# Kernel optimization log

Measured on AMD Instinct MI355X. Metric: run time of the kernel, lower is better.

## Reference

```python
import jax, jax.numpy as jnp
import numpy as np
from jax import lax

B, S, H, T = 64, 512, 1024, 67


def setup_inputs() -> dict:
    key = jax.random.key(0)
    ks = jax.random.split(key, 8)
    hidden = jax.random.normal(ks[0], (B, S, H), jnp.float32)
    labels = jax.random.randint(ks[1], (B, S), 0, T)
    lengths = jax.random.randint(ks[2], (B,), S // 2, S + 1)
    mask = (jnp.arange(S)[None, :] < lengths[:, None]).astype(jnp.int32)  # prefix mask, mask[:,0]=1
    W = jax.random.normal(ks[3], (H, T), jnp.float32) * 0.02
    b = jnp.zeros((T,), jnp.float32)
    start_trans = jax.random.uniform(ks[4], (T,), jnp.float32, -0.1, 0.1)
    end_trans = jax.random.uniform(ks[5], (T,), jnp.float32, -0.1, 0.1)
    trans = jax.random.uniform(ks[6], (T, T), jnp.float32, -0.1, 0.1)
    return dict(hidden=hidden, labels=labels, mask=mask, W=W, b=b,
                start_trans=start_trans, end_trans=end_trans, trans=trans)


def _crf_llh(em, tags, mask, start_trans, end_trans, trans):
    # em: (B,S,T), tags: (B,S) int, mask: (B,S) bool. torchcrf log-likelihood per sequence.
    maskf = mask.astype(em.dtype)
    # numerator: score of the gold path
    em_tag = jnp.take_along_axis(em, tags[:, :, None], axis=2)[:, :, 0]       # (B,S)
    num = start_trans[tags[:, 0]] + em_tag[:, 0]
    trans_tag = trans[tags[:, :-1], tags[:, 1:]]                              # (B,S-1)
    num = num + jnp.sum((trans_tag + em_tag[:, 1:]) * maskf[:, 1:], axis=1)
    last_idx = jnp.sum(mask.astype(jnp.int32), axis=1) - 1                    # (B,)
    last_tags = jnp.take_along_axis(tags, last_idx[:, None], axis=1)[:, 0]
    num = num + end_trans[last_tags]
    # denominator: log partition via forward algorithm (scan over time)
    def step(score, x):
        em_i, m_i = x  # (B,T), (B,)
        nxt = jax.nn.logsumexp(score[:, :, None] + trans[None] + em_i[:, None, :], axis=1)
        return jnp.where(m_i[:, None], nxt, score), None
    init = start_trans[None, :] + em[:, 0]
    score, _ = lax.scan(step, init, (em[:, 1:].transpose(1, 0, 2), mask[:, 1:].T))
    denom = jax.nn.logsumexp(score + end_trans[None, :], axis=1)
    return num - denom


def _viterbi(em, mask, start_trans, end_trans, trans):
    # returns best tag sequence (B,S), padded positions set to 0
    n_tags = em.shape[-1]
    ident = jnp.arange(n_tags)[None, :]
    def fwd(score, x):
        em_i, m_i = x  # (B,T), (B,)
        cand = score[:, :, None] + trans[None]                                # (B,T,T)
        idx = jnp.argmax(cand, axis=1)                                        # (B,T)
        nxt = jnp.max(cand, axis=1) + em_i
        score = jnp.where(m_i[:, None], nxt, score)
        idx = jnp.where(m_i[:, None], idx, ident)  # identity link on padded steps
        return score, idx
    init = start_trans[None, :] + em[:, 0]
    score, hist = lax.scan(fwd, init, (em[:, 1:].transpose(1, 0, 2), mask[:, 1:].T))
    best = jnp.argmax(score + end_trans[None, :], axis=1)                     # (B,)
    def back(carry, h):  # carry = tag at t+1, h = hist[t]: (B,T)
        prev = jnp.take_along_axis(h, carry[:, None], axis=1)[:, 0]
        return prev, prev
    _, ys = lax.scan(back, best, hist, reverse=True)                          # (S-1,B) tags[0..S-2]
    tags = jnp.concatenate([ys.transpose(1, 0), best[:, None]], axis=1)       # (B,S)
    return jnp.where(mask, tags, 0)


def reference(hidden, labels, mask, W, b, start_trans, end_trans, trans):
    maskb = mask.astype(bool)
    # dropout is identity in eval mode
    em = jnp.einsum('bsh,ht->bst', jax.nn.leaky_relu(hidden, 0.01), W) + b     # token_scores
    llh = _crf_llh(em, labels, maskb, start_trans, end_trans, trans)
    loss = -jnp.sum(llh) / em.shape[0]
    tags = _viterbi(em, maskb, start_trans, end_trans, trans)
    return loss, tags, em
```

## Files before the change

### kernel.cpp

```cpp
#include <hip/hip_runtime.h>

#define Bn 64
#define Sn 512
#define Hn 1024
#define Tn 67

#define LOG2E 1.4426950408889634f
#define LN2   0.6931471805599453f

__global__ __launch_bounds__(256) void gemm_em(
    const float* __restrict__ hidden, const float* __restrict__ W,
    const float* __restrict__ bias, float* __restrict__ em,
    float* __restrict__ out)
{
    __shared__ __align__(16) float hs[64][36];
    __shared__ __align__(16) float wt[80][36];

    const int tid = threadIdx.x;
    const int tx = tid & 15, ty = tid >> 4;
    const int row0 = blockIdx.x * 64;

    if (blockIdx.x == 0 && tid == 0) out[0] = 0.0f;

    float acc[4][5];
#pragma unroll
    for (int u = 0; u < 4; ++u)
#pragma unroll
        for (int v = 0; v < 5; ++v) acc[u][v] = 0.f;

    for (int kc = 0; kc < Hn; kc += 32) {
#pragma unroll
        for (int l = 0; l < 2; ++l) {
            int idx = tid + l * 256;
            int r = idx >> 3, kq = (idx & 7) << 2;
            float4 v = *reinterpret_cast<const float4*>(
                &hidden[(size_t)(row0 + r) * Hn + kc + kq]);
            v.x = v.x > 0.f ? v.x : 0.01f * v.x;
            v.y = v.y > 0.f ? v.y : 0.01f * v.y;
            v.z = v.z > 0.f ? v.z : 0.01f * v.z;
            v.w = v.w > 0.f ? v.w : 0.01f * v.w;
            *reinterpret_cast<float4*>(&hs[r][kq]) = v;
        }
        for (int idx = tid; idx < 32 * Tn; idx += 256) {
            int k = idx / Tn;
            int t = idx - k * Tn;
            wt[t][k] = W[(size_t)(kc + k) * Tn + t];
        }
        __syncthreads();

#pragma unroll
        for (int k0 = 0; k0 < 32; k0 += 4) {
            float4 hv[4], wv[5];
#pragma unroll
            for (int u = 0; u < 4; ++u)
                hv[u] = *reinterpret_cast<float4*>(&hs[ty + 16 * u][k0]);
#pragma unroll
            for (int v = 0; v < 5; ++v)
                wv[v] = *reinterpret_cast<float4*>(&wt[tx + 16 * v][k0]);
#pragma unroll
            for (int u = 0; u < 4; ++u)
#pragma unroll
                for (int v = 0; v < 5; ++v) {
                    acc[u][v] = fmaf(hv[u].x, wv[v].x, acc[u][v]);
                    acc[u][v] = fmaf(hv[u].y, wv[v].y, acc[u][v]);
                    acc[u][v] = fmaf(hv[u].z, wv[v].z, acc[u][v]);
                    acc[u][v] = fmaf(hv[u].w, wv[v].w, acc[u][v]);
                }
        }
        __syncthreads();
    }

#pragma unroll
    for (int v = 0; v < 5; ++v) {
        int c = tx + 16 * v;
        if (c < Tn) {
            float bb = bias[c];
#pragma unroll
            for (int u = 0; u < 4; ++u) {
                int row = row0 + ty + 16 * u;
                em[(size_t)row * Tn + c] = acc[u][v] + bb;
            }
        }
    }
}

__device__ __forceinline__ unsigned long long shflx64(unsigned long long v, int m) {
    unsigned int lo = (unsigned int)v, hi = (unsigned int)(v >> 32);
    lo = __shfl_xor(lo, m);
    hi = __shfl_xor(hi, m);
    return ((unsigned long long)hi << 32) | lo;
}

__device__ __forceinline__ unsigned long long packkey(float v, int idx) {
    unsigned int b = __float_as_uint(v);
    unsigned int s = b ^ (unsigned int)(((int)b >> 31) | 0x80000000);
    return ((unsigned long long)s << 32) | (unsigned int)(127 - idx);
}

__device__ __forceinline__ float unpackval(unsigned long long key) {
    unsigned int s = (unsigned int)(key >> 32);
    unsigned int b = s ^ (unsigned int)((~(int)s >> 31) | 0x80000000);
    return __uint_as_float(b);
}

__global__ __launch_bounds__(192) void crf_scan3(
    const float* __restrict__ em, const int* __restrict__ labels,
    const int* __restrict__ mask, const float* __restrict__ startT,
    const float* __restrict__ endT, const float* __restrict__ trans,
    float* __restrict__ out)
{
    __shared__ __align__(16) float emC[2][1088];
    __shared__ __align__(16) float emV[2][1088];
    __shared__ int maskC[Sn];
    __shared__ int maskV[Sn];
    __shared__ __align__(16) float pb[2][72];
    __shared__ __align__(16) float vb[2][72];
    __shared__ unsigned char hist[Sn - 1][68];
    __shared__ int tg[Sn];
    __shared__ float numSh;
    __shared__ int lenSh;

    const int tid = threadIdx.x;
    const int wid = tid >> 6;
    const int lane = tid & 63;
    const int b = blockIdx.x;
    const float* emg = em + (size_t)b * Sn * Tn;
    const int u2 = lane < 3 ? lane : 2;
    const int st2 = 64 + u2;

    if (wid == 0) {
#pragma unroll
        for (int i = 0; i < 8; ++i)
            maskC[lane + i * 64] = mask[b * Sn + lane + i * 64];

        float Ec1[68], Ec2[68];
#pragma unroll
        for (int i = 0; i < Tn; ++i) {
            Ec1[i] = exp2f(trans[i * Tn + lane] * LOG2E);
            Ec2[i] = exp2f(trans[i * Tn + st2] * LOG2E);
        }
        Ec1[67] = 0.f; Ec2[67] = 0.f;

        float sreg[17];
#pragma unroll
        for (int i = 0; i < 17; ++i) { int idx = lane + i * 64; if (idx > 1071) idx = 1071; sreg[i] = emg[idx]; }
#pragma unroll
        for (int i = 0; i < 17; ++i) {
            int idx = lane + i * 64;
            if (idx < 1072) { int s = idx / 67; emC[0][s * 68 + (idx - s * 67)] = sreg[i]; }
        }
#pragma unroll
        for (int i = 0; i < 17; ++i) { int idx = lane + i * 64; if (idx > 1071) idx = 1071; sreg[i] = emg[1072 + idx]; }

        if (lane == 0) { pb[0][67] = 0.f; pb[1][67] = 0.f; }

        float sc1 = startT[lane] + emC[0][lane];
        float sc2 = startT[st2] + emC[0][st2];
        float M = __shfl(sc1, 0);
        float p1 = exp2f((sc1 - M) * LOG2E);
        float p2 = exp2f((sc2 - M) * LOG2E);
        pb[0][lane] = p1;
        if (lane < 3) pb[0][64 + lane] = p2;
        float Mprev = M;

        for (int t = 1; t < Sn; ++t) {
            const int cb = (t >> 4) & 1;
            if ((t & 15) == 0) {
                const int k = t >> 4;
#pragma unroll
                for (int i = 0; i < 17; ++i) {
                    int idx = lane + i * 64;
                    if (idx < 1072) { int s = idx / 67; emC[cb][s * 68 + (idx - s * 67)] = sreg[i]; }
                }
                if (k < 31) {
                    const float* src = emg + (size_t)(k + 1) * 1072;
#pragma unroll
                    for (int i = 0; i < 17; ++i) { int idx = lane + i * 64; if (idx > 1071) idx = 1071; sreg[i] = src[idx]; }
                }
            }
            const float* row = &emC[cb][(t & 15) * 68];
            float em1 = row[lane];
            float em2 = row[st2];
            int m = maskC[t];
            const float4* P = (const float4*)&pb[(t + 1) & 1][0];
            float a0 = 0, a1 = 0, a2 = 0, a3 = 0, c0 = 0, c1 = 0, c2 = 0, c3 = 0;
#pragma unroll
            for (int q = 0; q < 17; ++q) {
                float4 pv = P[q];
                a0 = fmaf(pv.x, Ec1[4 * q + 0], a0); c0 = fmaf(pv.x, Ec2[4 * q + 0], c0);
                a1 = fmaf(pv.y, Ec1[4 * q + 1], a1); c1 = fmaf(pv.y, Ec2[4 * q + 1], c1);
                a2 = fmaf(pv.z, Ec1[4 * q + 2], a2); c2 = fmaf(pv.z, Ec2[4 * q + 2], c2);
                a3 = fmaf(pv.w, Ec1[4 * q + 3], a3); c3 = fmaf(pv.w, Ec2[4 * q + 3], c3);
            }
            float s1 = (a0 + a1) + (a2 + a3);
            float s2 = (c0 + c1) + (c2 + c3);
            float n1 = Mprev + log2f(s1) * LN2 + em1;
            float n2 = Mprev + log2f(s2) * LN2 + em2;
            if (m) { sc1 = n1; sc2 = n2; }
            M = __shfl(sc1, 0);
            p1 = exp2f((sc1 - M) * LOG2E);
            p2 = exp2f((sc2 - M) * LOG2E);
            float* Wp = &pb[t & 1][0];
            Wp[lane] = p1;
            if (lane < 3) Wp[64 + lane] = p2;
            Mprev = M;
        }

        float* F = &pb[0][0];
        F[lane] = sc1 + endT[lane];
        if (lane < 3) F[64 + lane] = sc2 + endT[64 + lane];
        if (lane == 0) F[67] = -1e30f;
        float mx = -1e30f;
        const float4* Fv = (const float4*)F;
#pragma unroll
        for (int q = 0; q < 17; ++q) {
            float4 v = Fv[q];
            mx = fmaxf(mx, fmaxf(fmaxf(v.x, v.y), fmaxf(v.z, v.w)));
        }
        float ss = 0.f;
#pragma unroll
        for (int q = 0; q < 17; ++q) {
            float4 v = Fv[q];
            ss += exp2f((v.x - mx) * LOG2E) + exp2f((v.y - mx) * LOG2E)
                + exp2f((v.z - mx) * LOG2E) + exp2f((v.w - mx) * LOG2E);
        }
        float denom = mx + log2f(ss) * LN2;
        __syncthreads();
        if (lane == 0) {
            int len = lenSh;
            float num = numSh + endT[labels[b * Sn + len - 1]];
            atomicAdd(out, -(num - denom) * (1.0f / (float)Bn));
        }
    } else if (wid == 1) {
#pragma unroll
        for (int i = 0; i < 8; ++i)
            maskV[lane + i * 64] = mask[b * Sn + lane + i * 64];

        float Tc1[68];
#pragma unroll
        for (int i = 0; i < Tn; ++i) Tc1[i] = trans[i * Tn + lane];
        Tc1[67] = 0.f;
        float Tsf[3], Tss[3];
        const int rsec = (lane < 3) ? (64 + lane) : 0;
#pragma unroll
        for (int u = 0; u < 3; ++u) {
            Tsf[u] = trans[lane * Tn + 64 + u];
            Tss[u] = trans[rsec * Tn + 64 + u];
        }

        float sreg[17];
#pragma unroll
        for (int i = 0; i < 17; ++i) { int idx = lane + i * 64; if (idx > 1071) idx = 1071; sreg[i] = emg[idx]; }
#pragma unroll
        for (int i = 0; i < 17; ++i) {
            int idx = lane + i * 64;
            if (idx < 1072) { int s = idx / 67; emV[0][s * 68 + (idx - s * 67)] = sreg[i]; }
        }
#pragma unroll
        for (int i = 0; i < 17; ++i) { int idx = lane + i * 64; if (idx > 1071) idx = 1071; sreg[i] = emg[1072 + idx]; }

        float sc1 = startT[lane] + emV[0][lane];
        float sc2 = startT[st2] + emV[0][st2];
        vb[0][lane] = sc1;
        if (lane < 3) vb[0][64 + lane] = sc2;
        if (lane == 0) { vb[0][67] = -1e30f; vb[1][67] = -1e30f; }

        for (int t = 1; t < Sn; ++t) {
            const int cb = (t >> 4) & 1;
            if ((t & 15) == 0) {
                const int k = t >> 4;
#pragma unroll
                for (int i = 0; i < 17; ++i) {
                    int idx = lane + i * 64;
                    if (idx < 1072) { int s = idx / 67; emV[cb][s * 68 + (idx - s * 67)] = sreg[i]; }
                }
                if (k < 31) {
                    const float* src = emg + (size_t)(k + 1) * 1072;
#pragma unroll
                    for (int i = 0; i < 17; ++i) { int idx = lane + i * 64; if (idx > 1071) idx = 1071; sreg[i] = src[idx]; }
                }
            }
            const float* row = &emV[cb][(t & 15) * 68];
            float em1 = row[lane];
            float e64 = row[64], e65 = row[65], e66 = row[66];
            int m = maskV[t];

            const float4* Vp = (const float4*)&vb[(t + 1) & 1][0];
            float bvv[34]; int bx[34];
#pragma unroll
            for (int q = 0; q < 17; ++q) {
                float4 v = Vp[q];
                float c0 = v.x + Tc1[4 * q + 0];
                float c1 = v.y + Tc1[4 * q + 1];
                float c2 = v.z + Tc1[4 * q + 2];
                float c3 = v.w + Tc1[4 * q + 3];
                bool r0 = c1 > c0;
                bvv[2 * q]     = r0 ? c1 : c0;
                bx[2 * q]      = r0 ? 4 * q + 1 : 4 * q + 0;
                bool r1 = c3 > c2;
                bvv[2 * q + 1] = r1 ? c3 : c2;
                bx[2 * q + 1]  = r1 ? 4 * q + 3 : 4 * q + 2;
            }
#pragma unroll
            for (int q = 0; q < 17; ++q) {
                bool r = bvv[2 * q + 1] > bvv[2 * q];
                bvv[q] = r ? bvv[2 * q + 1] : bvv[2 * q];
                bx[q]  = r ? bx[2 * q + 1]  : bx[2 * q];
            }
#pragma unroll
            for (int q = 0; q < 8; ++q) {
                bool r = bvv[2 * q + 1] > bvv[2 * q];
                bvv[q] = r ? bvv[2 * q + 1] : bvv[2 * q];
                bx[q]  = r ? bx[2 * q + 1]  : bx[2 * q];
            }
            bvv[8] = bvv[16]; bx[8] = bx[16];
#pragma unroll
            for (int q = 0; q < 4; ++q) {
                bool r = bvv[2 * q + 1] > bvv[2 * q];
                bvv[q] = r ? bvv[2 * q + 1] : bvv[2 * q];
                bx[q]  = r ? bx[2 * q + 1]  : bx[2 * q];
            }
            bvv[4] = bvv[8]; bx[4] = bx[8];
#pragma unroll
            for (int q = 0; q < 2; ++q) {
                bool r = bvv[2 * q + 1] > bvv[2 * q];
                bvv[q] = r ? bvv[2 * q + 1] : bvv[2 * q];
                bx[q]  = r ? bx[2 * q + 1]  : bx[2 * q];
            }
            bvv[2] = bvv[4]; bx[2] = bx[4];
            { bool r = bvv[1] > bvv[0]; bvv[0] = r ? bvv[1] : bvv[0]; bx[0] = r ? bx[1] : bx[0]; }
            { bool r = bvv[2] > bvv[0]; bvv[0] = r ? bvv[2] : bvv[0]; bx[0] = r ? bx[2] : bx[0]; }
            float n1 = bvv[0] + em1;

            float ca = sc1 + Tsf[0]; int ia = lane;
            float cbv = sc1 + Tsf[1]; int ib = lane;
            float cc = sc1 + Tsf[2]; int ic = lane;
            if (lane < 3) {
                float sa = sc2 + Tss[0]; if (sa > ca)  { ca = sa;  ia = 64 + lane; }
                float sb = sc2 + Tss[1]; if (sb > cbv) { cbv = sb; ib = 64 + lane; }
                float scv = sc2 + Tss[2]; if (scv > cc) { cc = scv; ic = 64 + lane; }
            }
            unsigned long long k0 = packkey(ca, ia);
            unsigned long long k1 = packkey(cbv, ib);
            unsigned long long k2 = packkey(cc, ic);
#pragma unroll
            for (int k = 1; k < 64; k <<= 1) {
                unsigned long long o0 = shflx64(k0, k); if (o0 > k0) k0 = o0;
                unsigned long long o1 = shflx64(k1, k); if (o1 > k1) k1 = o1;
                unsigned long long o2 = shflx64(k2, k); if (o2 > k2) k2 = o2;
            }
            float v64 = unpackval(k0) + e64;
            float v65 = unpackval(k1) + e65;
            float v66 = unpackval(k2) + e66;
            int i64 = 127 - (int)(unsigned int)(k0 & 0xffffffffu);
            int i65 = 127 - (int)(unsigned int)(k1 & 0xffffffffu);
            int i66 = 127 - (int)(unsigned int)(k2 & 0xffffffffu);

            float nuv = (lane == 0) ? v64 : (lane == 1) ? v65 : v66;
            int nui = (lane == 0) ? i64 : (lane == 1) ? i65 : i66;

            int idx1 = m ? bx[0] : lane;
            int idx2 = m ? nui : st2;
            if (m) { sc1 = n1; sc2 = nuv; }

            hist[t - 1][lane] = (unsigned char)idx1;
            float* Wv = &vb[t & 1][0];
            Wv[lane] = sc1;
            if (lane < 3) {
                hist[t - 1][64 + lane] = (unsigned char)idx2;
                Wv[64 + lane] = sc2;
            }
        }

        float* F = &vb[0][0];
        F[lane] = sc1 + endT[lane];
        if (lane < 3) F[64 + lane] = sc2 + endT[64 + lane];
        if (lane == 0) F[67] = -1e30f;
        const float4* Fv = (const float4*)F;
        float bvv[34]; int bx[34];
#pragma unroll
        for (int q = 0; q < 17; ++q) {
            float4 v = Fv[q];
            bool r0 = v.y > v.x;
            bvv[2 * q]     = r0 ? v.y : v.x;
            bx[2 * q]      = r0 ? 4 * q + 1 : 4 * q + 0;
            bool r1 = v.w > v.z;
            bvv[2 * q + 1] = r1 ? v.w : v.z;
            bx[2 * q + 1]  = r1 ? 4 * q + 3 : 4 * q + 2;
        }
#pragma unroll
        for (int q = 0; q < 17; ++q) {
            bool r = bvv[2 * q + 1] > bvv[2 * q];
            bvv[q] = r ? bvv[2 * q + 1] : bvv[2 * q];
            bx[q]  = r ? bx[2 * q + 1]  : bx[2 * q];
        }
#pragma unroll
        for (int q = 0; q < 8; ++q) {
            bool r = bvv[2 * q + 1] > bvv[2 * q];
            bvv[q] = r ? bvv[2 * q + 1] : bvv[2 * q];
            bx[q]  = r ? bx[2 * q + 1]  : bx[2 * q];
        }
        bvv[8] = bvv[16]; bx[8] = bx[16];
#pragma unroll
        for (int q = 0; q < 4; ++q) {
            bool r = bvv[2 * q + 1] > bvv[2 * q];
            bvv[q] = r ? bvv[2 * q + 1] : bvv[2 * q];
            bx[q]  = r ? bx[2 * q + 1]  : bx[2 * q];
        }
        bvv[4] = bvv[8]; bx[4] = bx[8];
#pragma unroll
        for (int q = 0; q < 2; ++q) {
            bool r = bvv[2 * q + 1] > bvv[2 * q];
            bvv[q] = r ? bvv[2 * q + 1] : bvv[2 * q];
            bx[q]  = r ? bx[2 * q + 1]  : bx[2 * q];
        }
        bvv[2] = bvv[4]; bx[2] = bx[4];
        { bool r = bvv[1] > bvv[0]; bvv[0] = r ? bvv[1] : bvv[0]; bx[0] = r ? bx[1] : bx[0]; }
        { bool r = bvv[2] > bvv[0]; bvv[0] = r ? bvv[2] : bvv[0]; bx[0] = r ? bx[2] : bx[0]; }

        if (lane == 0) {
            int carry = bx[0];
            tg[Sn - 1] = carry;
            for (int k = Sn - 2; k >= 0; --k) {
                carry = hist[k][carry];
                tg[k] = carry;
            }
        }
        float* tagsOut = out + 1 + b * Sn;
#pragma unroll
        for (int i = 0; i < 8; ++i) {
            int s = lane + i * 64;
            tagsOut[s] = maskV[s] ? (float)tg[s] : 0.f;
        }
        __syncthreads();
    } else {
        float part = 0.f; int lenp = 0;
#pragma unroll
        for (int i = 0; i < 8; ++i) {
            int s = lane + i * 64;
            int ms = mask[b * Sn + s];
            lenp += ms;
            int ls = labels[b * Sn + s];
            if (s == 0) {
                part += startT[ls] + emg[ls];
            } else if (ms) {
                int lp = labels[b * Sn + s - 1];
                part += trans[lp * Tn + ls] + emg[(size_t)s * Tn + ls];
            }
        }
#pragma unroll
        for (int k = 1; k < 64; k <<= 1) {
            part += __shfl_xor(part, k);
            lenp += __shfl_xor(lenp, k);
        }
        if (lane == 0) { numSh = part; lenSh = lenp; }
        __syncthreads();
    }
}

extern "C" void kernel_launch(void* const* d_in, const int* in_sizes, int n_in,
                              void* d_out, int out_size, void* d_ws, size_t ws_size,
                              hipStream_t stream) {
    const float* hidden = (const float*)d_in[0];
    const int*   labels = (const int*)d_in[1];
    const int*   maskp  = (const int*)d_in[2];
    const float* W      = (const float*)d_in[3];
    const float* bias   = (const float*)d_in[4];
    const float* startT = (const float*)d_in[5];
    const float* endT   = (const float*)d_in[6];
    const float* trans  = (const float*)d_in[7];
    float* out = (float*)d_out;
    float* em  = out + 1 + (size_t)Bn * Sn;

    hipLaunchKernelGGL(gemm_em, dim3((Bn * Sn) / 64), dim3(256), 0, stream,
                       hidden, W, bias, em, out);
    hipLaunchKernelGGL(crf_scan3, dim3(Bn), dim3(192), 0, stream,
                       em, labels, maskp, startT, endT, trans, out);
}
```

Before: 789.6 us.

## Transpose tail-tag work in CRF scans via shared gather buffers, drop shuffle reductions

The forward and Viterbi recurrences each handled tags 64..66 per lane (forward) or through 64-bit packed-key wave shuffles (Viterbi). Now every lane writes its score combined with the three tail transition columns into small shared buffers, and lanes 0-2 reduce one buffer row. This removes the per-step shuffle butterfly and halves the register tables. The forward pass also replaces the wave-broadcast max normalizer with a running log-sum normalizer computed from the summed probabilities, removing one shuffle per step. In exchange it adds more shared-memory writes per step, and the new normalizer can drift numerically.

```diff
diff --git a/kernel.cpp b/kernel.cpp
--- a/kernel.cpp
+++ b/kernel.cpp
@@ -84,26 +84,102 @@
     }
 }
 
-__device__ __forceinline__ unsigned long long shflx64(unsigned long long v, int m) {
-    unsigned int lo = (unsigned int)v, hi = (unsigned int)(v >> 32);
-    lo = __shfl_xor(lo, m);
-    hi = __shfl_xor(hi, m);
-    return ((unsigned long long)hi << 32) | lo;
+__device__ __forceinline__ void tmax68_add(const float4* Vp, const float* T,
+                                           float& bv, int& bi)
+{
+    float bvv[34]; int bx[34];
+#pragma unroll
+    for (int q = 0; q < 17; ++q) {
+        float4 v = Vp[q];
+        float c0 = v.x + T[4 * q + 0];
+        float c1 = v.y + T[4 * q + 1];
+        float c2 = v.z + T[4 * q + 2];
+        float c3 = v.w + T[4 * q + 3];
+        bool r0 = c1 > c0;
+        bvv[2 * q]     = r0 ? c1 : c0;
+        bx[2 * q]      = r0 ? 4 * q + 1 : 4 * q + 0;
+        bool r1 = c3 > c2;
+        bvv[2 * q + 1] = r1 ? c3 : c2;
+        bx[2 * q + 1]  = r1 ? 4 * q + 3 : 4 * q + 2;
+    }
+#pragma unroll
+    for (int q = 0; q < 17; ++q) {
+        bool r = bvv[2 * q + 1] > bvv[2 * q];
+        bvv[q] = r ? bvv[2 * q + 1] : bvv[2 * q];
+        bx[q]  = r ? bx[2 * q + 1]  : bx[2 * q];
+    }
+#pragma unroll
+    for (int q = 0; q < 8; ++q) {
+        bool r = bvv[2 * q + 1] > bvv[2 * q];
+        bvv[q] = r ? bvv[2 * q + 1] : bvv[2 * q];
+        bx[q]  = r ? bx[2 * q + 1]  : bx[2 * q];
+    }
+    bvv[8] = bvv[16]; bx[8] = bx[16];
+#pragma unroll
+    for (int q = 0; q < 4; ++q) {
+        bool r = bvv[2 * q + 1] > bvv[2 * q];
+        bvv[q] = r ? bvv[2 * q + 1] : bvv[2 * q];
+        bx[q]  = r ? bx[2 * q + 1]  : bx[2 * q];
+    }
+    bvv[4] = bvv[8]; bx[4] = bx[8];
+#pragma unroll
+    for (int q = 0; q < 2; ++q) {
+        bool r = bvv[2 * q + 1] > bvv[2 * q];
+        bvv[q] = r ? bvv[2 * q + 1] : bvv[2 * q];
+        bx[q]  = r ? bx[2 * q + 1]  : bx[2 * q];
+    }
+    bvv[2] = bvv[4]; bx[2] = bx[4];
+    { bool r = bvv[1] > bvv[0]; bvv[0] = r ? bvv[1] : bvv[0]; bx[0] = r ? bx[1] : bx[0]; }
+    { bool r = bvv[2] > bvv[0]; bvv[0] = r ? bvv[2] : bvv[0]; bx[0] = r ? bx[2] : bx[0]; }
+    bv = bvv[0]; bi = bx[0];
 }
 
-__device__ __forceinline__ unsigned long long packkey(float v, int idx) {
-    unsigned int b = __float_as_uint(v);
-    unsigned int s = b ^ (unsigned int)(((int)b >> 31) | 0x80000000);
-    return ((unsigned long long)s << 32) | (unsigned int)(127 - idx);
+__device__ __forceinline__ void tmax68_plain(const float4* Vp, float& bv, int& bi)
+{
+    float bvv[34]; int bx[34];
+#pragma unroll
+    for (int q = 0; q < 17; ++q) {
+        float4 v = Vp[q];
+        bool r0 = v.y > v.x;
+        bvv[2 * q]     = r0 ? v.y : v.x;
+        bx[2 * q]      = r0 ? 4 * q + 1 : 4 * q + 0;
+        bool r1 = v.w > v.z;
+        bvv[2 * q + 1] = r1 ? v.w : v.z;
+        bx[2 * q + 1]  = r1 ? 4 * q + 3 : 4 * q + 2;
+    }
+#pragma unroll
+    for (int q = 0; q < 17; ++q) {
+        bool r = bvv[2 * q + 1] > bvv[2 * q];
+        bvv[q] = r ? bvv[2 * q + 1] : bvv[2 * q];
+        bx[q]  = r ? bx[2 * q + 1]  : bx[2 * q];
+    }
+#pragma unroll
+    for (int q = 0; q < 8; ++q) {
+        bool r = bvv[2 * q + 1] > bvv[2 * q];
+        bvv[q] = r ? bvv[2 * q + 1] : bvv[2 * q];
+        bx[q]  = r ? bx[2 * q + 1]  : bx[2 * q];
+    }
+    bvv[8] = bvv[16]; bx[8] = bx[16];
+#pragma unroll
+    for (int q = 0; q < 4; ++q) {
+        bool r = bvv[2 * q + 1] > bvv[2 * q];
+        bvv[q] = r ? bvv[2 * q + 1] : bvv[2 * q];
+        bx[q]  = r ? bx[2 * q + 1]  : bx[2 * q];
+    }
+    bvv[4] = bvv[8]; bx[4] = bx[8];
+#pragma unroll
+    for (int q = 0; q < 2; ++q) {
+        bool r = bvv[2 * q + 1] > bvv[2 * q];
+        bvv[q] = r ? bvv[2 * q + 1] : bvv[2 * q];
+        bx[q]  = r ? bx[2 * q + 1]  : bx[2 * q];
+    }
+    bvv[2] = bvv[4]; bx[2] = bx[4];
+    { bool r = bvv[1] > bvv[0]; bvv[0] = r ? bvv[1] : bvv[0]; bx[0] = r ? bx[1] : bx[0]; }
+    { bool r = bvv[2] > bvv[0]; bvv[0] = r ? bvv[2] : bvv[0]; bx[0] = r ? bx[2] : bx[0]; }
+    bv = bvv[0]; bi = bx[0];
 }
 
-__device__ __forceinline__ float unpackval(unsigned long long key) {
-    unsigned int s = (unsigned int)(key >> 32);
-    unsigned int b = s ^ (unsigned int)((~(int)s >> 31) | 0x80000000);
-    return __uint_as_float(b);
-}
-
-__global__ __launch_bounds__(192) void crf_scan3(
+__global__ __launch_bounds__(192) void crf_scan4(
     const float* __restrict__ em, const int* __restrict__ labels,
     const int* __restrict__ mask, const float* __restrict__ startT,
     const float* __restrict__ endT, const float* __restrict__ trans,
@@ -114,7 +190,9 @@
     __shared__ int maskC[Sn];
     __shared__ int maskV[Sn];
     __shared__ __align__(16) float pb[2][72];
+    __shared__ __align__(16) float gC[2][3][72];
     __shared__ __align__(16) float vb[2][72];
+    __shared__ __align__(16) float gV[2][3][72];
     __shared__ unsigned char hist[Sn - 1][68];
     __shared__ int tg[Sn];
     __shared__ float numSh;
@@ -133,13 +211,16 @@
         for (int i = 0; i < 8; ++i)
             maskC[lane + i * 64] = mask[b * Sn + lane + i * 64];
 
-        float Ec1[68], Ec2[68];
-#pragma unroll
-        for (int i = 0; i < Tn; ++i) {
-            Ec1[i] = exp2f(trans[i * Tn + lane] * LOG2E);
-            Ec2[i] = exp2f(trans[i * Tn + st2] * LOG2E);
-        }
-        Ec1[67] = 0.f; Ec2[67] = 0.f;
+        float Ec1[68];
+#pragma unroll
+        for (int i = 0; i < Tn; ++i) Ec1[i] = exp2f(trans[i * Tn + lane] * LOG2E);
+        Ec1[67] = 0.f;
+        float Esf[3], Ess[3];
+#pragma unroll
+        for (int u = 0; u < 3; ++u) {
+            Esf[u] = exp2f(trans[lane * Tn + 64 + u] * LOG2E);
+            Ess[u] = exp2f(trans[st2 * Tn + 64 + u] * LOG2E);
+        }
 
         float sreg[17];
 #pragma unroll
@@ -152,16 +233,25 @@
 #pragma unroll
         for (int i = 0; i < 17; ++i) { int idx = lane + i * 64; if (idx > 1071) idx = 1071; sreg[i] = emg[1072 + idx]; }
 
-        if (lane == 0) { pb[0][67] = 0.f; pb[1][67] = 0.f; }
+        if (lane == 0) {
+            pb[0][67] = 0.f; pb[1][67] = 0.f;
+#pragma unroll
+            for (int u = 0; u < 3; ++u) { gC[0][u][67] = 0.f; gC[1][u][67] = 0.f; }
+        }
 
         float sc1 = startT[lane] + emC[0][lane];
         float sc2 = startT[st2] + emC[0][st2];
-        float M = __shfl(sc1, 0);
+        float M = startT[0] + emC[0][0];
         float p1 = exp2f((sc1 - M) * LOG2E);
         float p2 = exp2f((sc2 - M) * LOG2E);
         pb[0][lane] = p1;
         if (lane < 3) pb[0][64 + lane] = p2;
-        float Mprev = M;
+#pragma unroll
+        for (int u = 0; u < 3; ++u) gC[0][u][lane] = p1 * Esf[u];
+        if (lane < 3) {
+#pragma unroll
+            for (int v = 0; v < 3; ++v) gC[0][v][64 + lane] = p2 * Ess[v];
+        }
 
         for (int t = 1; t < Sn; ++t) {
             const int cb = (t >> 4) & 1;
@@ -178,32 +268,50 @@
                     for (int i = 0; i < 17; ++i) { int idx = lane + i * 64; if (idx > 1071) idx = 1071; sreg[i] = src[idx]; }
                 }
             }
+            const int pv = (t + 1) & 1, cu = t & 1;
             const float* row = &emC[cb][(t & 15) * 68];
             float em1 = row[lane];
             float em2 = row[st2];
             int m = maskC[t];
-            const float4* P = (const float4*)&pb[(t + 1) & 1][0];
-            float a0 = 0, a1 = 0, a2 = 0, a3 = 0, c0 = 0, c1 = 0, c2 = 0, c3 = 0;
+
+            const float4* P = (const float4*)&pb[pv][0];
+            float a0 = 0, a1 = 0, a2 = 0, a3 = 0;
+            float s0 = 0, s1s = 0, s2s = 0, s3 = 0;
 #pragma unroll
             for (int q = 0; q < 17; ++q) {
-                float4 pv = P[q];
-                a0 = fmaf(pv.x, Ec1[4 * q + 0], a0); c0 = fmaf(pv.x, Ec2[4 * q + 0], c0);
-                a1 = fmaf(pv.y, Ec1[4 * q + 1], a1); c1 = fmaf(pv.y, Ec2[4 * q + 1], c1);
-                a2 = fmaf(pv.z, Ec1[4 * q + 2], a2); c2 = fmaf(pv.z, Ec2[4 * q + 2], c2);
-                a3 = fmaf(pv.w, Ec1[4 * q + 3], a3); c3 = fmaf(pv.w, Ec2[4 * q + 3], c3);
-            }
-            float s1 = (a0 + a1) + (a2 + a3);
-            float s2 = (c0 + c1) + (c2 + c3);
-            float n1 = Mprev + log2f(s1) * LN2 + em1;
-            float n2 = Mprev + log2f(s2) * LN2 + em2;
+                float4 pvv = P[q];
+                a0 = fmaf(pvv.x, Ec1[4 * q + 0], a0);
+                a1 = fmaf(pvv.y, Ec1[4 * q + 1], a1);
+                a2 = fmaf(pvv.z, Ec1[4 * q + 2], a2);
+                a3 = fmaf(pvv.w, Ec1[4 * q + 3], a3);
+                s0 += pvv.x; s1s += pvv.y; s2s += pvv.z; s3 += pvv.w;
+            }
+            float aa1 = (a0 + a1) + (a2 + a3);
+            float S = (s0 + s1s) + (s2s + s3);
+
+            const float4* G = (const float4*)&gC[pv][u2][0];
+            float g0 = 0, g1 = 0, g2 = 0, g3 = 0;
+#pragma unroll
+            for (int q = 0; q < 17; ++q) {
+                float4 gv = G[q];
+                g0 += gv.x; g1 += gv.y; g2 += gv.z; g3 += gv.w;
+            }
+            float aa2 = (g0 + g1) + (g2 + g3);
+
+            float n1 = M + log2f(aa1) * LN2 + em1;
+            float n2 = M + log2f(aa2) * LN2 + em2;
             if (m) { sc1 = n1; sc2 = n2; }
-            M = __shfl(sc1, 0);
+            M = M + log2f(S) * LN2;
             p1 = exp2f((sc1 - M) * LOG2E);
             p2 = exp2f((sc2 - M) * LOG2E);
-            float* Wp = &pb[t & 1][0];
-            Wp[lane] = p1;
-            if (lane < 3) Wp[64 + lane] = p2;
-            Mprev = M;
+            pb[cu][lane] = p1;
+            if (lane < 3) pb[cu][64 + lane] = p2;
+#pragma unroll
+            for (int u = 0; u < 3; ++u) gC[cu][u][lane] = p1 * Esf[u];
+            if (lane < 3) {
+#pragma unroll
+                for (int v = 0; v < 3; ++v) gC[cu][v][64 + lane] = p2 * Ess[v];
+            }
         }
 
         float* F = &pb[0][0];
@@ -241,11 +349,10 @@
         for (int i = 0; i < Tn; ++i) Tc1[i] = trans[i * Tn + lane];
         Tc1[67] = 0.f;
         float Tsf[3], Tss[3];
-        const int rsec = (lane < 3) ? (64 + lane) : 0;
 #pragma unroll
         for (int u = 0; u < 3; ++u) {
             Tsf[u] = trans[lane * Tn + 64 + u];
-            Tss[u] = trans[rsec * Tn + 64 + u];
+            Tss[u] = trans[st2 * Tn + 64 + u];
         }
 
         float sreg[17];
@@ -258,12 +365,23 @@
         }
 #pragma unroll
         for (int i = 0; i < 17; ++i) { int idx = lane + i * 64; if (idx > 1071) idx = 1071; sreg[i] = emg[1072 + idx]; }
+
+        if (lane == 0) {
+            vb[0][67] = -1e30f; vb[1][67] = -1e30f;
+#pragma unroll
+            for (int u = 0; u < 3; ++u) { gV[0][u][67] = -1e30f; gV[1][u][67] = -1e30f; }
+        }
 
         float sc1 = startT[lane] + emV[0][lane];
         float sc2 = startT[st2] + emV[0][st2];
         vb[0][lane] = sc1;
         if (lane < 3) vb[0][64 + lane] = sc2;
-        if (lane == 0) { vb[0][67] = -1e30f; vb[1][67] = -1e30f; }
+#pragma unroll
+        for (int u = 0; u < 3; ++u) gV[0][u][lane] = sc1 + Tsf[u];
+        if (lane < 3) {
+#pragma unroll
+            for (int v = 0; v < 3; ++v) gV[0][v][64 + lane] = sc2 + Tss[v];
+        }
 
         for (int t = 1; t < Sn; ++t) {
             const int cb = (t >> 4) & 1;
@@ -280,95 +398,33 @@
                     for (int i = 0; i < 17; ++i) { int idx = lane + i * 64; if (idx > 1071) idx = 1071; sreg[i] = src[idx]; }
                 }
             }
+            const int pv = (t + 1) & 1, cu = t & 1;
             const float* row = &emV[cb][(t & 15) * 68];
             float em1 = row[lane];
-            float e64 = row[64], e65 = row[65], e66 = row[66];
+            float em2 = row[st2];
             int m = maskV[t];
 
-            const float4* Vp = (const float4*)&vb[(t + 1) & 1][0];
-            float bvv[34]; int bx[34];
-#pragma unroll
-            for (int q = 0; q < 17; ++q) {
-                float4 v = Vp[q];
-                float c0 = v.x + Tc1[4 * q + 0];
-                float c1 = v.y + Tc1[4 * q + 1];
-                float c2 = v.z + Tc1[4 * q + 2];
-                float c3 = v.w + Tc1[4 * q + 3];
-                bool r0 = c1 > c0;
-                bvv[2 * q]     = r0 ? c1 : c0;
-                bx[2 * q]      = r0 ? 4 * q + 1 : 4 * q + 0;
-                bool r1 = c3 > c2;
-                bvv[2 * q + 1] = r1 ? c3 : c2;
-                bx[2 * q + 1]  = r1 ? 4 * q + 3 : 4 * q + 2;
-            }
-#pragma unroll
-            for (int q = 0; q < 17; ++q) {
-                bool r = bvv[2 * q + 1] > bvv[2 * q];
-                bvv[q] = r ? bvv[2 * q + 1] : bvv[2 * q];
-                bx[q]  = r ? bx[2 * q + 1]  : bx[2 * q];
-            }
-#pragma unroll
-            for (int q = 0; q < 8; ++q) {
-                bool r = bvv[2 * q + 1] > bvv[2 * q];
-                bvv[q] = r ? bvv[2 * q + 1] : bvv[2 * q];
-                bx[q]  = r ? bx[2 * q + 1]  : bx[2 * q];
-            }
-            bvv[8] = bvv[16]; bx[8] = bx[16];
-#pragma unroll
-            for (int q = 0; q < 4; ++q) {
-                bool r = bvv[2 * q + 1] > bvv[2 * q];
-                bvv[q] = r ? bvv[2 * q + 1] : bvv[2 * q];
-                bx[q]  = r ? bx[2 * q + 1]  : bx[2 * q];
-            }
-            bvv[4] = bvv[8]; bx[4] = bx[8];
-#pragma unroll
-            for (int q = 0; q < 2; ++q) {
-                bool r = bvv[2 * q + 1] > bvv[2 * q];
-                bvv[q] = r ? bvv[2 * q + 1] : bvv[2 * q];
-                bx[q]  = r ? bx[2 * q + 1]  : bx[2 * q];
-            }
-            bvv[2] = bvv[4]; bx[2] = bx[4];
-            { bool r = bvv[1] > bvv[0]; bvv[0] = r ? bvv[1] : bvv[0]; bx[0] = r ? bx[1] : bx[0]; }
-            { bool r = bvv[2] > bvv[0]; bvv[0] = r ? bvv[2] : bvv[0]; bx[0] = r ? bx[2] : bx[0]; }
-            float n1 = bvv[0] + em1;
-
-            float ca = sc1 + Tsf[0]; int ia = lane;
-            float cbv = sc1 + Tsf[1]; int ib = lane;
-            float cc = sc1 + Tsf[2]; int ic = lane;
-            if (lane < 3) {
-                float sa = sc2 + Tss[0]; if (sa > ca)  { ca = sa;  ia = 64 + lane; }
-                float sb = sc2 + Tss[1]; if (sb > cbv) { cbv = sb; ib = 64 + lane; }
-                float scv = sc2 + Tss[2]; if (scv > cc) { cc = scv; ic = 64 + lane; }
-            }
-            unsigned long long k0 = packkey(ca, ia);
-            unsigned long long k1 = packkey(cbv, ib);
-            unsigned long long k2 = packkey(cc, ic);
-#pragma unroll
-            for (int k = 1; k < 64; k <<= 1) {
-                unsigned long long o0 = shflx64(k0, k); if (o0 > k0) k0 = o0;
-                unsigned long long o1 = shflx64(k1, k); if (o1 > k1) k1 = o1;
-                unsigned long long o2 = shflx64(k2, k); if (o2 > k2) k2 = o2;
-            }
-            float v64 = unpackval(k0) + e64;
-            float v65 = unpackval(k1) + e65;
-            float v66 = unpackval(k2) + e66;
-            int i64 = 127 - (int)(unsigned int)(k0 & 0xffffffffu);
-            int i65 = 127 - (int)(unsigned int)(k1 & 0xffffffffu);
-            int i66 = 127 - (int)(unsigned int)(k2 & 0xffffffffu);
-
-            float nuv = (lane == 0) ? v64 : (lane == 1) ? v65 : v66;
-            int nui = (lane == 0) ? i64 : (lane == 1) ? i65 : i66;
-
-            int idx1 = m ? bx[0] : lane;
-            int idx2 = m ? nui : st2;
-            if (m) { sc1 = n1; sc2 = nuv; }
+            float bv1; int bi1;
+            tmax68_add((const float4*)&vb[pv][0], Tc1, bv1, bi1);
+            float n1 = bv1 + em1;
+
+            float bv2; int bi2;
+            tmax68_plain((const float4*)&gV[pv][u2][0], bv2, bi2);
+            float n2 = bv2 + em2;
+
+            int idx1 = m ? bi1 : lane;
+            int idx2 = m ? bi2 : st2;
+            if (m) { sc1 = n1; sc2 = n2; }
 
             hist[t - 1][lane] = (unsigned char)idx1;
-            float* Wv = &vb[t & 1][0];
-            Wv[lane] = sc1;
+            vb[cu][lane] = sc1;
+#pragma unroll
+            for (int u = 0; u < 3; ++u) gV[cu][u][lane] = sc1 + Tsf[u];
             if (lane < 3) {
                 hist[t - 1][64 + lane] = (unsigned char)idx2;
-                Wv[64 + lane] = sc2;
+                vb[cu][64 + lane] = sc2;
+#pragma unroll
+                for (int v = 0; v < 3; ++v) gV[cu][v][64 + lane] = sc2 + Tss[v];
             }
         }
 
@@ -376,50 +432,11 @@
         F[lane] = sc1 + endT[lane];
         if (lane < 3) F[64 + lane] = sc2 + endT[64 + lane];
         if (lane == 0) F[67] = -1e30f;
-        const float4* Fv = (const float4*)F;
-        float bvv[34]; int bx[34];
-#pragma unroll
-        for (int q = 0; q < 17; ++q) {
-            float4 v = Fv[q];
-            bool r0 = v.y > v.x;
-            bvv[2 * q]     = r0 ? v.y : v.x;
-            bx[2 * q]      = r0 ? 4 * q + 1 : 4 * q + 0;
-            bool r1 = v.w > v.z;
-            bvv[2 * q + 1] = r1 ? v.w : v.z;
-            bx[2 * q + 1]  = r1 ? 4 * q + 3 : 4 * q + 2;
-        }
-#pragma unroll
-        for (int q = 0; q < 17; ++q) {
-            bool r = bvv[2 * q + 1] > bvv[2 * q];
-            bvv[q] = r ? bvv[2 * q + 1] : bvv[2 * q];
-            bx[q]  = r ? bx[2 * q + 1]  : bx[2 * q];
-        }
-#pragma unroll
-        for (int q = 0; q < 8; ++q) {
-            bool r = bvv[2 * q + 1] > bvv[2 * q];
-            bvv[q] = r ? bvv[2 * q + 1] : bvv[2 * q];
-            bx[q]  = r ? bx[2 * q + 1]  : bx[2 * q];
-        }
-        bvv[8] = bvv[16]; bx[8] = bx[16];
-#pragma unroll
-        for (int q = 0; q < 4; ++q) {
-            bool r = bvv[2 * q + 1] > bvv[2 * q];
-            bvv[q] = r ? bvv[2 * q + 1] : bvv[2 * q];
-            bx[q]  = r ? bx[2 * q + 1]  : bx[2 * q];
-        }
-        bvv[4] = bvv[8]; bx[4] = bx[8];
-#pragma unroll
-        for (int q = 0; q < 2; ++q) {
-            bool r = bvv[2 * q + 1] > bvv[2 * q];
-            bvv[q] = r ? bvv[2 * q + 1] : bvv[2 * q];
-            bx[q]  = r ? bx[2 * q + 1]  : bx[2 * q];
-        }
-        bvv[2] = bvv[4]; bx[2] = bx[4];
-        { bool r = bvv[1] > bvv[0]; bvv[0] = r ? bvv[1] : bvv[0]; bx[0] = r ? bx[1] : bx[0]; }
-        { bool r = bvv[2] > bvv[0]; bvv[0] = r ? bvv[2] : bvv[0]; bx[0] = r ? bx[2] : bx[0]; }
+        float bvf; int bif;
+        tmax68_plain((const float4*)F, bvf, bif);
 
         if (lane == 0) {
-            int carry = bx[0];
+            int carry = bif;
             tg[Sn - 1] = carry;
             for (int k = Sn - 2; k >= 0; --k) {
                 carry = hist[k][carry];
@@ -474,6 +491,6 @@
 
     hipLaunchKernelGGL(gemm_em, dim3((Bn * Sn) / 64), dim3(256), 0, stream,
                        hidden, W, bias, em, out);
-    hipLaunchKernelGGL(crf_scan3, dim3(Bn), dim3(192), 0, stream,
+    hipLaunchKernelGGL(crf_scan4, dim3(Bn), dim3(192), 0, stream,
                        em, labels, maskp, startT, endT, trans, out);
 }
```

Measured after the change: 988.8 us. +25.2%, slower.
